# Kernel tuning notes

Hardware: AMD Instinct MI355X
Metric: run time of the kernel (lower is better)

Reference implementation:

```python
import jax, jax.numpy as jnp
import numpy as np

N, D, A, NQ, G1, G2 = 2048, 512, 64, 8, 8, 8
A1 = 2 * A  # tier-1 MQA uses att_dim*2 internally


def setup_inputs() -> dict:
    key = jax.random.key(0)
    ks = iter(jax.random.split(key, 24))
    r = lambda *sh: (jax.random.normal(next(ks), sh, dtype=jnp.float32) * 0.02)
    return {
        "x": jax.random.normal(next(ks), (N, D), dtype=jnp.float32),
        # tier 1 (num_groups_first MQA blocks, inner dim A1)
        "Wq1": r(G1, NQ, D, A1), "bq1": r(G1, NQ, A1),
        "Wk1": r(G1, D, A1),     "bk1": r(G1, A1),
        "Wv1": r(G1, D, A1),     "bv1": r(G1, A1),
        "Wo1": r(G1, NQ * A1, D), "bo1": r(G1, D),
        # tier 2 (num_groups_second MQA blocks, inner dim A)
        "Wq2": r(G2, NQ, D, A), "bq2": r(G2, NQ, A),
        "Wk2": r(G2, D, A),     "bk2": r(G2, A),
        "Wv2": r(G2, D, A),     "bv2": r(G2, A),
        "Wo2": r(G2, NQ * A, D), "bo2": r(G2, D),
        # final projection: in = att_dim * num_groups_second == D
        "Wo": r(D, D), "bo": r(D),
    }


def _mqa_grouped(xg, Wq, bq, Wk, bk, Wv, bv, Wo, bo):
    """Batched MultiQueryAttention over a group axis g.
    xg: [g, n, d]; Wq: [g, q, d, a]. No softmax (per source)."""
    a = Wq.shape[-1]
    q = jnp.einsum('gnd,gqda->gqna', xg, Wq) + bq[:, :, None, :]
    k = jnp.einsum('gnd,gda->gna', xg, Wk) + bk[:, None, :]
    v = jnp.einsum('gnd,gda->gna', xg, Wv) + bv[:, None, :]
    scores = jnp.einsum('gqna,gma->gqnm', q, k) / jnp.sqrt(jnp.asarray(a, jnp.float32))
    ctx = jnp.einsum('gqnm,gma->gqna', scores, v)          # [g,q,n,a]
    g, nq, n, ad = ctx.shape
    ctx = ctx.transpose(0, 2, 1, 3).reshape(g, n, nq * ad)  # concat queries on feat dim
    return jnp.einsum('gnf,gfd->gnd', ctx, Wo) + bo[:, None, :]


def reference(x, Wq1, bq1, Wk1, bk1, Wv1, bv1, Wo1, bo1,
              Wq2, bq2, Wk2, bk2, Wv2, bv2, Wo2, bo2, Wo, bo):
    xg = jnp.broadcast_to(x[None], (G1, N, D))
    o1 = _mqa_grouped(xg, Wq1, bq1, Wk1, bk1, Wv1, bv1, Wo1, bo1)   # [G1,N,D]
    o2 = _mqa_grouped(o1[:G2], Wq2, bq2, Wk2, bk2, Wv2, bv2, Wo2, bo2)  # [G2,N,D]
    o2_flat = o2.reshape(G2 * N, D)  # torch.cat along token dim (dim=0)
    return o2_flat @ Wo + bo          # [G2*N, D]
```

## Files before the change

### kernel.cpp

```cpp
#include <hip/hip_runtime.h>


typedef __bf16 bf16x8 __attribute__((ext_vector_type(8)));
typedef float  f32x4  __attribute__((ext_vector_type(4)));

struct PD { const float* s; void* d; int R, C, Bc, mode, blocks; };
struct PArgs { PD p[20]; int n; };

struct MA {
    const float *x,*bq1,*bo1,*bq2,*bo2,*bo;
    float* out;
    __bf16 *xb,*Wk1t,*Wv1t,*Wq1b,*Wo1t,*Wk2t,*Wv2t,*Wq2b,*Wo2b,*Wot;
    __bf16 *Ktb,*Vtb,*T1b,*M1t,*o1b,*K2tb,*V2tb,*T2b,*Wo2pT,*M2pt;
    float *STf1,*STf2,*kvb1,*kvb2,*c1,*c2p,*bo2p;
    PArgs pa;
    int prepTot;
};

template<int BM, int BN, bool BF32>
__device__ __forceinline__ void gemm_block(void* smv,
    const __bf16* __restrict__ A, const void* __restrict__ Bv,
    const float* __restrict__ bias, void* __restrict__ Cv,
    int K, int lda, int ldb, int ldc, int divq, int ksplit,
    long aOut, long aIn, long bOut, long bIn, long cOut, long cIn,
    long biasOut, long biasIn, int hasBias, int mode, float alpha,
    int bx, int by, int bz)
{
    constexpr int MT = BM / 32, NT = BN / 32;
    __bf16 (*As)[32] = (__bf16(*)[32])smv;
    __bf16 (*Bs)[32] = (__bf16(*)[32])((char*)smv + BM * 64);

    int b  = bz / ksplit, ks = bz - b * ksplit;
    int go = b / divq,  gi = b - go * divq;
    A += go * aOut + gi * aIn;
    const __bf16* Bb = (const __bf16*)Bv + (BF32 ? 0 : (go * bOut + gi * bIn));
    const float*  Bf = (const float*)Bv + (BF32 ? (go * bOut + gi * bIn) : 0);
    long cBase = go * cOut + gi * cIn;
    if (hasBias) bias += go * biasOut + gi * biasIn;

    int kChunk = K / ksplit;
    int k0 = ks * kChunk, kEnd = k0 + kChunk;

    int bm = by * BM, bn = bx * BN;
    int tid = threadIdx.x, wave = tid >> 6, lane = tid & 63;
    int wm = (wave >> 1) * (BM / 2), wn = (wave & 1) * (BN / 2);
    int mrow = lane & 15, quad = lane >> 4;

    f32x4 acc[MT][NT];
    #pragma unroll
    for (int i = 0; i < MT; ++i)
        #pragma unroll
        for (int j = 0; j < NT; ++j)
            acc[i][j] = f32x4{0.f, 0.f, 0.f, 0.f};

    for (; k0 < kEnd; k0 += 32) {
        __syncthreads();
        #pragma unroll
        for (int t = 0; t < BM / 64; ++t) {
            int c = tid + t * 256;
            int row = c >> 2, kq = c & 3;
            __builtin_amdgcn_global_load_lds(
                (const __attribute__((address_space(1))) void*)
                    (A + (long)(bm + row) * lda + k0 + kq * 8),
                (__attribute__((address_space(3))) void*)&As[row][kq * 8],
                16, 0, 0);
        }
        if (!BF32) {
            #pragma unroll
            for (int t = 0; t < BN / 64; ++t) {
                int c = tid + t * 256;
                int row = c >> 2, kq = c & 3;
                __builtin_amdgcn_global_load_lds(
                    (const __attribute__((address_space(1))) void*)
                        (Bb + (long)(bn + row) * ldb + k0 + kq * 8),
                    (__attribute__((address_space(3))) void*)&Bs[row][kq * 8],
                    16, 0, 0);
            }
        } else {
            int row = tid >> 2, cb = (tid & 3) * 8;
            const float* src = Bf + (long)(bn + row) * ldb + k0 + cb;
            float4 f0 = *(const float4*)(src);
            float4 f1 = *(const float4*)(src + 4);
            bf16x8 v = {(__bf16)f0.x, (__bf16)f0.y, (__bf16)f0.z, (__bf16)f0.w,
                        (__bf16)f1.x, (__bf16)f1.y, (__bf16)f1.z, (__bf16)f1.w};
            *(bf16x8*)&Bs[row][cb] = v;
        }
        __syncthreads();

        bf16x8 af[MT], bfv[NT];
        #pragma unroll
        for (int mt = 0; mt < MT; ++mt)
            af[mt] = *(const bf16x8*)&As[wm + mt * 16 + mrow][quad * 8];
        #pragma unroll
        for (int nt = 0; nt < NT; ++nt)
            bfv[nt] = *(const bf16x8*)&Bs[wn + nt * 16 + mrow][quad * 8];
        #pragma unroll
        for (int mt = 0; mt < MT; ++mt)
            #pragma unroll
            for (int nt = 0; nt < NT; ++nt)
                acc[mt][nt] = __builtin_amdgcn_mfma_f32_16x16x32_bf16(
                    af[mt], bfv[nt], acc[mt][nt], 0, 0, 0);
    }

    #pragma unroll
    for (int mt = 0; mt < MT; ++mt) {
        #pragma unroll
        for (int r = 0; r < 4; ++r) {
            int row = bm + wm + mt * 16 + quad * 4 + r;
            #pragma unroll
            for (int nt = 0; nt < NT; ++nt) {
                int col = bn + wn + nt * 16 + mrow;
                float v = acc[mt][nt][r] * alpha;
                if (hasBias) v += bias[col];
                if (mode == 0)
                    ((float*)Cv)[cBase + (long)row * ldc + col] = v;
                else if (mode == 1)
                    ((__bf16*)Cv)[cBase + (long)row * ldc + col] = (__bf16)v;
                else if (mode == 2)
                    ((__bf16*)Cv)[cBase + (long)col * ldc + row] = (__bf16)v;
                else
                    atomicAdd(&((float*)Cv)[cBase + (long)row * ldc + col], v);
            }
        }
    }
}

__device__ __forceinline__ void prep_block(const PArgs& a, int bid, void* smv)
{
    int i = 0;
    while (i < a.n && bid >= a.p[i].blocks) { bid -= a.p[i].blocks; ++i; }
    if (i >= a.n) return;
    PD d = a.p[i];
    int t = threadIdx.x;
    if (d.mode == 0) {
        float (*tile)[33] = (float(*)[33])smv;
        int tC = d.C >> 5, tR = d.R >> 5;
        int batch = bid / (tC * tR), rem = bid - batch * (tC * tR);
        int tyo = rem / tC, txo = rem - tyo * tC;
        const float* src = d.s + (long)batch * d.R * d.C;
        __bf16* dst = (__bf16*)d.d + (long)batch * d.R * d.C;
        int tx = t & 31, ty = t >> 5;
        int r0 = tyo * 32, c0 = txo * 32;
        #pragma unroll
        for (int u = 0; u < 4; ++u)
            tile[ty + 8 * u][tx] = src[(long)(r0 + ty + 8 * u) * d.C + c0 + tx];
        __syncthreads();
        #pragma unroll
        for (int u = 0; u < 4; ++u)
            dst[(long)(c0 + ty + 8 * u) * d.R + r0 + tx] = (__bf16)tile[tx][ty + 8 * u];
    } else if (d.mode == 1) {
        long idx = ((long)bid * 256 + t) * 4;
        long total = (long)d.Bc * d.R * d.C;
        if (idx < total) {
            float4 f = *(const float4*)(d.s + idx);
            __bf16* o = (__bf16*)d.d + idx;
            o[0] = (__bf16)f.x; o[1] = (__bf16)f.y;
            o[2] = (__bf16)f.z; o[3] = (__bf16)f.w;
        }
    } else {
        long idx = (long)bid * 256 + t;
        long total = (long)d.Bc * d.R * d.C;
        if (idx < total) {
            float* o = (float*)d.d;
            if (d.mode == 2) o[idx] = d.s[idx];
            else             o[idx] = 0.f;
        }
    }
}

__device__ __forceinline__ void small_block(void* smv,
    const float* __restrict__ STf, const float* __restrict__ bq,
    const __bf16* __restrict__ WoT, const float* __restrict__ boA,
    float* __restrict__ cOut, int ad, int F, long wG, int bid)
{
    int tid = threadIdx.x;
    float* rL  = (float*)smv;
    float* red = (float*)((char*)smv + 4096);
    int g = bid >> 5, slice = bid & 31;
    int nq = F / ad;
    const float* Sg = STf + (long)g * ad * ad;
    for (int f = tid; f < F; f += 256) {
        int q = f / ad, aa = f - q * ad;
        const float* bv = bq + (long)(g * nq + q) * ad;
        const float* Sa = Sg + (long)aa * ad;
        float s = 0.f;
        for (int c = 0; c < ad; c += 4) {
            float4 b4 = *(const float4*)(bv + c);
            float4 s4 = *(const float4*)(Sa + c);
            s += b4.x * s4.x + b4.y * s4.y + b4.z * s4.z + b4.w * s4.w;
        }
        rL[f] = s;
    }
    __syncthreads();
    int dl = tid & 15, fs = tid >> 4;
    int d = slice * 16 + dl;
    int fchunk = F >> 4;
    const __bf16* wrow = WoT + (long)g * wG + (long)d * F;
    float s = 0.f;
    for (int f0 = fs * fchunk; f0 < (fs + 1) * fchunk; f0 += 8) {
        bf16x8 w = *(const bf16x8*)(wrow + f0);
        s += rL[f0]     * (float)w[0] + rL[f0 + 1] * (float)w[1]
           + rL[f0 + 2] * (float)w[2] + rL[f0 + 3] * (float)w[3]
           + rL[f0 + 4] * (float)w[4] + rL[f0 + 5] * (float)w[5]
           + rL[f0 + 6] * (float)w[6] + rL[f0 + 7] * (float)w[7];
    }
    red[tid] = s;
    __syncthreads();
    if (fs == 0) {
        float tsum = s;
        #pragma unroll
        for (int u = 1; u < 16; ++u) tsum += red[u * 16 + dl];
        cOut[(long)g * 512 + d] = boA[(long)g * 512 + d] + tsum;
    }
}

__device__ __forceinline__ void vecmat_block(void* smv,
    const float* __restrict__ v, const __bf16* __restrict__ WT,
    const float* __restrict__ bias, float* __restrict__ outp, int g, int slice)
{
    float* red2 = (float*)smv;
    int tid = threadIdx.x;
    int dl = tid & 15, fs = tid >> 4;
    int d = slice * 16 + dl;
    const float* vg = v + (long)g * 512;
    const __bf16* wrow = WT + (long)d * 512;
    float s = 0.f;
    for (int f0 = fs * 32; f0 < (fs + 1) * 32; f0 += 8) {
        bf16x8 w = *(const bf16x8*)(wrow + f0);
        s += vg[f0]     * (float)w[0] + vg[f0 + 1] * (float)w[1]
           + vg[f0 + 2] * (float)w[2] + vg[f0 + 3] * (float)w[3]
           + vg[f0 + 4] * (float)w[4] + vg[f0 + 5] * (float)w[5]
           + vg[f0 + 6] * (float)w[6] + vg[f0 + 7] * (float)w[7];
    }
    red2[tid] = s;
    __syncthreads();
    if (fs == 0) {
        float tsum = s;
        #pragma unroll
        for (int u = 1; u < 16; ++u) tsum += red2[u * 16 + dl];
        outp[(long)g * 512 + d] = bias[d] + tsum;
    }
}

__device__ __forceinline__ void run_stage(const MA& a, int s, int vb, void* sm)
{
    const float isa1 = 0.08838834764831845f;
    switch (s) {
    case 0: prep_block(a.pa, vb, sm); break;
    case 1:
        if (vb < 1024)
            gemm_block<64,64,false>(sm, a.xb, a.Wk1t, a.kvb1, a.Ktb,
                512, 512, 512, 2048, 1, 1,
                0L, 0L, 65536L, 0L, 262144L, 0L, 128L, 0L, 1, 2, 1.0f,
                vb & 1, (vb >> 1) & 31, vb >> 6);
        else if (vb < 1536) {
            int v = vb - 1024;
            gemm_block<64,64,false>(sm, a.Wo2b, a.Wot, nullptr, a.Wo2pT,
                512, 512, 512, 512, 1, 1,
                262144L, 0L, 0L, 0L, 262144L, 0L, 0L, 0L, 0, 2, 1.0f,
                v & 7, (v >> 3) & 7, v >> 6);
        } else {
            int v = vb - 1536;
            vecmat_block(sm, a.bo2, a.Wot, a.bo, a.bo2p, v & 7, v >> 3);
        }
        break;
    case 2:
        gemm_block<64,64,false>(sm, a.Vtb, a.Ktb, nullptr, a.STf1,
            2048, 2048, 2048, 128, 1, 8,
            262144L, 0L, 262144L, 0L, 16384L, 0L, 0L, 0L, 0, 3, isa1,
            vb & 1, (vb >> 1) & 1, vb >> 2);
        break;
    case 3:
        if (vb < 1024)
            gemm_block<64,64,true>(sm, a.Wq1b, a.STf1, nullptr, a.T1b,
                128, 128, 128, 1024, 8, 1,
                524288L, 65536L, 16384L, 0L, 524288L, 128L, 0L, 0L, 0, 1, 1.0f,
                vb & 1, (vb >> 1) & 7, vb >> 4);
        else
            small_block(sm, a.STf1, a.bq1, a.Wo1t, a.bo1, a.c1,
                        128, 1024, 524288L, vb - 1024);
        break;
    case 4:
        gemm_block<64,64,false>(sm, a.T1b, a.Wo1t, nullptr, a.M1t,
            1024, 1024, 1024, 512, 1, 1,
            524288L, 0L, 524288L, 0L, 262144L, 0L, 0L, 0L, 0, 2, 1.0f,
            vb & 7, (vb >> 3) & 7, vb >> 6);
        break;
    case 5:
        gemm_block<128,128,false>(sm, a.xb, a.M1t, a.c1, a.o1b,
            512, 512, 512, 512, 1, 1,
            0L, 0L, 262144L, 0L, 1048576L, 0L, 512L, 0L, 1, 1, 1.0f,
            vb & 3, (vb >> 2) & 15, vb >> 6);
        break;
    case 6:
        gemm_block<64,64,false>(sm, a.o1b, a.Wk2t, a.kvb2, a.K2tb,
            512, 512, 512, 2048, 8, 1,
            0L, 1048576L, 262144L, 32768L, 1048576L, 131072L, 512L, 64L,
            1, 2, 1.0f, 0, vb & 31, vb >> 5);
        break;
    case 7:
        gemm_block<64,64,false>(sm, a.V2tb, a.K2tb, nullptr, a.STf2,
            2048, 2048, 2048, 64, 1, 16,
            131072L, 0L, 131072L, 0L, 4096L, 0L, 0L, 0L, 0, 3, 0.125f,
            0, 0, vb);
        break;
    case 8:
        if (vb < 512)
            gemm_block<64,64,true>(sm, a.Wq2b, a.STf2, nullptr, a.T2b,
                64, 64, 64, 512, 8, 1,
                262144L, 32768L, 4096L, 0L, 262144L, 64L, 0L, 0L, 0, 1, 1.0f,
                0, vb & 7, vb >> 3);
        else
            small_block(sm, a.STf2, a.bq2, a.Wo2pT, a.bo2p, a.c2p,
                        64, 512, 262144L, vb - 512);
        break;
    case 9:
        gemm_block<64,64,false>(sm, a.T2b, a.Wo2pT, nullptr, a.M2pt,
            512, 512, 512, 512, 1, 1,
            262144L, 0L, 262144L, 0L, 262144L, 0L, 0L, 0L, 0, 2, 1.0f,
            vb & 7, (vb >> 3) & 7, vb >> 6);
        break;
    default:
        gemm_block<128,128,false>(sm, a.o1b, a.M2pt, a.c2p, a.out,
            512, 512, 512, 512, 1, 1,
            1048576L, 0L, 262144L, 0L, 1048576L, 0L, 512L, 0L, 1, 0, 1.0f,
            vb & 3, (vb >> 2) & 15, vb >> 6);
        break;
    }
}

__global__ __launch_bounds__(256, 4) void stage_kernel(MA a, int stage)
{
    __shared__ __align__(16) unsigned char smem[16384];
    run_stage(a, stage, blockIdx.x, smem);
}

extern "C" void kernel_launch(void* const* d_in, const int* in_sizes, int n_in,
                              void* d_out, int out_size, void* d_ws, size_t ws_size,
                              hipStream_t stream)
{
    MA ma;
    ma.x   = (const float*)d_in[0];
    const float* Wq1 = (const float*)d_in[1];  ma.bq1 = (const float*)d_in[2];
    const float* Wk1 = (const float*)d_in[3];  const float* bk1 = (const float*)d_in[4];
    const float* Wv1 = (const float*)d_in[5];  const float* bv1 = (const float*)d_in[6];
    const float* Wo1 = (const float*)d_in[7];  ma.bo1 = (const float*)d_in[8];
    const float* Wq2 = (const float*)d_in[9];  ma.bq2 = (const float*)d_in[10];
    const float* Wk2 = (const float*)d_in[11]; const float* bk2 = (const float*)d_in[12];
    const float* Wv2 = (const float*)d_in[13]; const float* bv2 = (const float*)d_in[14];
    const float* Wo2 = (const float*)d_in[15]; ma.bo2 = (const float*)d_in[16];
    const float* Wo  = (const float*)d_in[17]; ma.bo  = (const float*)d_in[18];
    ma.out = (float*)d_out;
    (void)in_sizes; (void)n_in; (void)out_size; (void)ws_size;

    __bf16* wb = (__bf16*)d_ws;
    long o = 0;
    ma.xb    = wb + o; o += 1048576;
    ma.Wk1t  = wb + o; o += 524288;
    ma.Wv1t  = wb + o; o += 524288;
    ma.Wq1b  = wb + o; o += 4194304;
    ma.Wo1t  = wb + o; o += 4194304;
    ma.Wk2t  = wb + o; o += 262144;
    ma.Wv2t  = wb + o; o += 262144;
    ma.Wq2b  = wb + o; o += 2097152;
    ma.Wo2b  = wb + o; o += 2097152;
    ma.Wot   = wb + o; o += 262144;
    ma.Ktb   = wb + o; o += 2097152;
    ma.Vtb   = wb + o; o += 2097152;
    ma.T1b   = wb + o; o += 4194304;
    ma.M1t   = wb + o; o += 2097152;
    ma.o1b   = wb + o; o += 8388608;
    ma.K2tb  = ma.Ktb;
    ma.V2tb  = ma.Ktb + 1048576;
    ma.T2b   = wb + o; o += 2097152;
    ma.Wo2pT = wb + o; o += 2097152;
    ma.M2pt  = wb + o; o += 2097152;
    float* wf = (float*)(wb + o);
    long p = 0;
    ma.STf1 = wf + p; p += 131072;
    ma.STf2 = wf + p; p += 32768;
    ma.kvb1 = wf + p; p += 2048;
    ma.kvb2 = wf + p; p += 1024;
    ma.c1   = wf + p; p += 4096;
    ma.c2p  = wf + p; p += 4096;
    ma.bo2p = wf + p; p += 4096;

    int nd = 0, totB = 0;
    auto add = [&](const float* s, void* d, int R, int C, int Bc, int mode) {
        int blocks;
        long total = (long)Bc * R * C;
        if (mode == 0) blocks = Bc * (R >> 5) * (C >> 5);
        else if (mode == 1) blocks = (int)(total / 1024);
        else blocks = (int)((total + 255) / 256);
        ma.pa.p[nd] = PD{s, d, R, C, Bc, mode, blocks};
        ++nd; totB += blocks;
    };
    add(ma.x, ma.xb,   2048, 512, 1, 1);
    add(Wq1,  ma.Wq1b, 512, 128, 64, 1);
    add(Wq2,  ma.Wq2b, 512, 64, 64, 1);
    add(Wo2,  ma.Wo2b, 512, 512, 8, 1);
    add(Wk1,  ma.Wk1t, 512, 128, 8, 0);
    add(Wv1,  ma.Wv1t, 512, 128, 8, 0);
    add(Wo1,  ma.Wo1t, 1024, 512, 8, 0);
    add(Wk2,  ma.Wk2t, 512, 64, 8, 0);
    add(Wv2,  ma.Wv2t, 512, 64, 8, 0);
    add(Wo,   ma.Wot,  512, 512, 1, 0);
    add(bk1,  ma.kvb1,        1, 1024, 1, 2);
    add(bv1,  ma.kvb1 + 1024, 1, 1024, 1, 2);
    add(bk2,  ma.kvb2,        1, 512, 1, 2);
    add(bv2,  ma.kvb2 + 512,  1, 512, 1, 2);
    add(nullptr, ma.STf1, 1, 131072, 1, 4);
    add(nullptr, ma.STf2, 1, 32768, 1, 4);
    ma.pa.n = nd;
    ma.prepTot = totB;

    const int counts[11] = {ma.prepTot, 1792, 256, 1280, 512, 512, 512, 128,
                            768, 512, 512};
    for (int s = 0; s < 11; ++s)
        stage_kernel<<<dim3(counts[s]), dim3(256), 0, stream>>>(ma, s);
}
```

Before: 301.6 us.

## Double-buffer GEMM LDS tiles and specialise stage kernels per template

The GEMM main loop now uses two shared-memory buffers. The next K-slice is issued with global_load_lds (plus register prefetch for the fp32 B path) while MFMAs run on the current slice, and explicit vmcnt/lgkmcnt waits and barriers order the two. The stage switch becomes a template parameter, so each launch compiles only its own stage and sizes LDS per stage, doubling it to 32KB for the 128x128 stages. This is meant to hide global-load latency and remove the switch dispatch, at the cost of more LDS per block, which may lower occupancy in the big tiles.

Measured after the change: 281.0 us. 1.07x faster.

```diff
diff --git a/kernel.cpp b/kernel.cpp
--- a/kernel.cpp
+++ b/kernel.cpp
@@ -27,8 +27,12 @@
     int bx, int by, int bz)
 {
     constexpr int MT = BM / 32, NT = BN / 32;
-    __bf16 (*As)[32] = (__bf16(*)[32])smv;
-    __bf16 (*Bs)[32] = (__bf16(*)[32])((char*)smv + BM * 64);
+    constexpr int HALF = (BM + BN) * 64;
+    constexpr int AL = BM / 64;
+    constexpr int BL = BF32 ? 0 : BN / 64;
+    constexpr int VTOT = AL + BL + (BF32 ? 2 : 0);
+
+    char* smc = (char*)smv;
 
     int b  = bz / ksplit, ks = bz - b * ksplit;
     int go = b / divq,  gi = b - go * divq;
@@ -39,7 +43,8 @@
     if (hasBias) bias += go * biasOut + gi * biasIn;
 
     int kChunk = K / ksplit;
-    int k0 = ks * kChunk, kEnd = k0 + kChunk;
+    int k0 = ks * kChunk;
+    int nT = kChunk / 32;
 
     int bm = by * BM, bn = bx * BN;
     int tid = threadIdx.x, wave = tid >> 6, lane = tid & 63;
@@ -53,53 +58,91 @@
         for (int j = 0; j < NT; ++j)
             acc[i][j] = f32x4{0.f, 0.f, 0.f, 0.f};
 
-    for (; k0 < kEnd; k0 += 32) {
-        __syncthreads();
-        #pragma unroll
-        for (int t = 0; t < BM / 64; ++t) {
+    float4 bf0, bf1;
+    int brow = tid >> 2, bcb = (tid & 3) * 8;
+
+    auto loadBf32 = [&](int kk) {
+        const float* src = Bf + (long)(bn + brow) * ldb + kk + bcb;
+        bf0 = *(const float4*)(src);
+        bf1 = *(const float4*)(src + 4);
+    };
+    auto writeBf32 = [&](int buf) {
+        bf16x8 v = {(__bf16)bf0.x, (__bf16)bf0.y, (__bf16)bf0.z, (__bf16)bf0.w,
+                    (__bf16)bf1.x, (__bf16)bf1.y, (__bf16)bf1.z, (__bf16)bf1.w};
+        *(bf16x8*)(smc + buf * HALF + BM * 64 + brow * 64 + bcb * 2) = v;
+    };
+    auto issueAB = [&](int buf, int kk) {
+        char* base = smc + buf * HALF;
+        #pragma unroll
+        for (int t = 0; t < AL; ++t) {
             int c = tid + t * 256;
             int row = c >> 2, kq = c & 3;
             __builtin_amdgcn_global_load_lds(
                 (const __attribute__((address_space(1))) void*)
-                    (A + (long)(bm + row) * lda + k0 + kq * 8),
-                (__attribute__((address_space(3))) void*)&As[row][kq * 8],
+                    (A + (long)(bm + row) * lda + kk + kq * 8),
+                (__attribute__((address_space(3))) void*)(base + row * 64 + kq * 16),
                 16, 0, 0);
         }
-        if (!BF32) {
+        if constexpr (!BF32) {
             #pragma unroll
-            for (int t = 0; t < BN / 64; ++t) {
+            for (int t = 0; t < BL; ++t) {
                 int c = tid + t * 256;
                 int row = c >> 2, kq = c & 3;
                 __builtin_amdgcn_global_load_lds(
                     (const __attribute__((address_space(1))) void*)
-                        (Bb + (long)(bn + row) * ldb + k0 + kq * 8),
-                    (__attribute__((address_space(3))) void*)&Bs[row][kq * 8],
+                        (Bb + (long)(bn + row) * ldb + kk + kq * 8),
+                    (__attribute__((address_space(3))) void*)
+                        (base + BM * 64 + row * 64 + kq * 16),
                     16, 0, 0);
             }
+        }
+    };
+
+    if constexpr (BF32) loadBf32(k0);
+    issueAB(0, k0);
+    if constexpr (BF32) {
+        writeBf32(0);
+        asm volatile("s_waitcnt lgkmcnt(0)" ::: "memory");
+        __builtin_amdgcn_sched_barrier(0);
+    }
+
+    int cur = 0;
+    for (int t = 0; t < nT; ++t) {
+        int kk = k0 + (t + 1) * 32;
+        if (t + 1 < nT) {
+            if constexpr (BF32) loadBf32(kk);
+            issueAB(cur ^ 1, kk);
+            asm volatile("s_waitcnt vmcnt(%0)" :: "n"(VTOT) : "memory");
         } else {
-            int row = tid >> 2, cb = (tid & 3) * 8;
-            const float* src = Bf + (long)(bn + row) * ldb + k0 + cb;
-            float4 f0 = *(const float4*)(src);
-            float4 f1 = *(const float4*)(src + 4);
-            bf16x8 v = {(__bf16)f0.x, (__bf16)f0.y, (__bf16)f0.z, (__bf16)f0.w,
-                        (__bf16)f1.x, (__bf16)f1.y, (__bf16)f1.z, (__bf16)f1.w};
-            *(bf16x8*)&Bs[row][cb] = v;
-        }
-        __syncthreads();
-
+            asm volatile("s_waitcnt vmcnt(0)" ::: "memory");
+        }
+        __builtin_amdgcn_sched_barrier(0);
+        __builtin_amdgcn_s_barrier();
+        __builtin_amdgcn_sched_barrier(0);
+
+        char* base = smc + cur * HALF;
         bf16x8 af[MT], bfv[NT];
         #pragma unroll
         for (int mt = 0; mt < MT; ++mt)
-            af[mt] = *(const bf16x8*)&As[wm + mt * 16 + mrow][quad * 8];
+            af[mt] = *(const bf16x8*)(base + (wm + mt * 16 + mrow) * 64 + quad * 16);
         #pragma unroll
         for (int nt = 0; nt < NT; ++nt)
-            bfv[nt] = *(const bf16x8*)&Bs[wn + nt * 16 + mrow][quad * 8];
+            bfv[nt] = *(const bf16x8*)(base + BM * 64 + (wn + nt * 16 + mrow) * 64 + quad * 16);
         #pragma unroll
         for (int mt = 0; mt < MT; ++mt)
             #pragma unroll
             for (int nt = 0; nt < NT; ++nt)
                 acc[mt][nt] = __builtin_amdgcn_mfma_f32_16x16x32_bf16(
                     af[mt], bfv[nt], acc[mt][nt], 0, 0, 0);
+
+        if constexpr (BF32) {
+            if (t + 1 < nT) writeBf32(cur ^ 1);
+        }
+
+        asm volatile("s_waitcnt lgkmcnt(0)" ::: "memory");
+        __builtin_amdgcn_sched_barrier(0);
+        __builtin_amdgcn_s_barrier();
+        cur ^= 1;
     }
 
     #pragma unroll
@@ -242,12 +285,13 @@
     }
 }
 
-__device__ __forceinline__ void run_stage(const MA& a, int s, int vb, void* sm)
+template<int S>
+__device__ __forceinline__ void run_stage(const MA& a, int vb, void* sm)
 {
     const float isa1 = 0.08838834764831845f;
-    switch (s) {
-    case 0: prep_block(a.pa, vb, sm); break;
-    case 1:
+    if constexpr (S == 0) {
+        prep_block(a.pa, vb, sm);
+    } else if constexpr (S == 1) {
         if (vb < 1024)
             gemm_block<64,64,false>(sm, a.xb, a.Wk1t, a.kvb1, a.Ktb,
                 512, 512, 512, 2048, 1, 1,
@@ -263,14 +307,12 @@
             int v = vb - 1536;
             vecmat_block(sm, a.bo2, a.Wot, a.bo, a.bo2p, v & 7, v >> 3);
         }
-        break;
-    case 2:
+    } else if constexpr (S == 2) {
         gemm_block<64,64,false>(sm, a.Vtb, a.Ktb, nullptr, a.STf1,
             2048, 2048, 2048, 128, 1, 8,
             262144L, 0L, 262144L, 0L, 16384L, 0L, 0L, 0L, 0, 3, isa1,
             vb & 1, (vb >> 1) & 1, vb >> 2);
-        break;
-    case 3:
+    } else if constexpr (S == 3) {
         if (vb < 1024)
             gemm_block<64,64,true>(sm, a.Wq1b, a.STf1, nullptr, a.T1b,
                 128, 128, 128, 1024, 8, 1,
@@ -279,32 +321,27 @@
         else
             small_block(sm, a.STf1, a.bq1, a.Wo1t, a.bo1, a.c1,
                         128, 1024, 524288L, vb - 1024);
-        break;
-    case 4:
+    } else if constexpr (S == 4) {
         gemm_block<64,64,false>(sm, a.T1b, a.Wo1t, nullptr, a.M1t,
             1024, 1024, 1024, 512, 1, 1,
             524288L, 0L, 524288L, 0L, 262144L, 0L, 0L, 0L, 0, 2, 1.0f,
             vb & 7, (vb >> 3) & 7, vb >> 6);
-        break;
-    case 5:
+    } else if constexpr (S == 5) {
         gemm_block<128,128,false>(sm, a.xb, a.M1t, a.c1, a.o1b,
             512, 512, 512, 512, 1, 1,
             0L, 0L, 262144L, 0L, 1048576L, 0L, 512L, 0L, 1, 1, 1.0f,
             vb & 3, (vb >> 2) & 15, vb >> 6);
-        break;
-    case 6:
+    } else if constexpr (S == 6) {
         gemm_block<64,64,false>(sm, a.o1b, a.Wk2t, a.kvb2, a.K2tb,
             512, 512, 512, 2048, 8, 1,
             0L, 1048576L, 262144L, 32768L, 1048576L, 131072L, 512L, 64L,
             1, 2, 1.0f, 0, vb & 31, vb >> 5);
-        break;
-    case 7:
+    } else if constexpr (S == 7) {
         gemm_block<64,64,false>(sm, a.V2tb, a.K2tb, nullptr, a.STf2,
             2048, 2048, 2048, 64, 1, 16,
             131072L, 0L, 131072L, 0L, 4096L, 0L, 0L, 0L, 0, 3, 0.125f,
             0, 0, vb);
-        break;
-    case 8:
+    } else if constexpr (S == 8) {
         if (vb < 512)
             gemm_block<64,64,true>(sm, a.Wq2b, a.STf2, nullptr, a.T2b,
                 64, 64, 64, 512, 8, 1,
@@ -313,26 +350,28 @@
         else
             small_block(sm, a.STf2, a.bq2, a.Wo2pT, a.bo2p, a.c2p,
                         64, 512, 262144L, vb - 512);
-        break;
-    case 9:
+    } else if constexpr (S == 9) {
         gemm_block<64,64,false>(sm, a.T2b, a.Wo2pT, nullptr, a.M2pt,
             512, 512, 512, 512, 1, 1,
             262144L, 0L, 262144L, 0L, 262144L, 0L, 0L, 0L, 0, 2, 1.0f,
             vb & 7, (vb >> 3) & 7, vb >> 6);
-        break;
-    default:
+    } else {
         gemm_block<128,128,false>(sm, a.o1b, a.M2pt, a.c2p, a.out,
             512, 512, 512, 512, 1, 1,
             1048576L, 0L, 262144L, 0L, 1048576L, 0L, 512L, 0L, 1, 0, 1.0f,
             vb & 3, (vb >> 2) & 15, vb >> 6);
-        break;
-    }
-}
-
-__global__ __launch_bounds__(256, 4) void stage_kernel(MA a, int stage)
-{
-    __shared__ __align__(16) unsigned char smem[16384];
-    run_stage(a, stage, blockIdx.x, smem);
+    }
+}
+
+constexpr int smem_bytes(int s) {
+    return (s == 5 || s == 10) ? 32768 : 16384;
+}
+
+template<int S>
+__global__ __launch_bounds__(256, 4) void stage_kernel(MA a)
+{
+    __shared__ __align__(16) unsigned char smem[smem_bytes(S)];
+    run_stage<S>(a, blockIdx.x, smem);
 }
 
 extern "C" void kernel_launch(void* const* d_in, const int* in_sizes, int n_in,
@@ -414,8 +453,15 @@
     ma.pa.n = nd;
     ma.prepTot = totB;
 
-    const int counts[11] = {ma.prepTot, 1792, 256, 1280, 512, 512, 512, 128,
-                            768, 512, 512};
-    for (int s = 0; s < 11; ++s)
-        stage_kernel<<<dim3(counts[s]), dim3(256), 0, stream>>>(ma, s);
-}
+    stage_kernel<0><<<dim3(ma.prepTot), dim3(256), 0, stream>>>(ma);
+    stage_kernel<1><<<dim3(1792), dim3(256), 0, stream>>>(ma);
+    stage_kernel<2><<<dim3(256),  dim3(256), 0, stream>>>(ma);
+    stage_kernel<3><<<dim3(1280), dim3(256), 0, stream>>>(ma);
+    stage_kernel<4><<<dim3(512),  dim3(256), 0, stream>>>(ma);
+    stage_kernel<5><<<dim3(512),  dim3(256), 0, stream>>>(ma);
+    stage_kernel<6><<<dim3(512),  dim3(256), 0, stream>>>(ma);
+    stage_kernel<7><<<dim3(128),  dim3(256), 0, stream>>>(ma);
+    stage_kernel<8><<<dim3(768),  dim3(256), 0, stream>>>(ma);
+    stage_kernel<9><<<dim3(512),  dim3(256), 0, stream>>>(ma);
+    stage_kernel<10><<<dim3(512), dim3(256), 0, stream>>>(ma);
+}
```
